# Kernel optimization log

Measured on AMD Instinct MI355X. Metric: run time of the kernel, lower is better.

The kernel has to match this reference:

```python
import jax, jax.numpy as jnp
import numpy as np

D_MODEL = 512
B, S = 8, 1024
NEG_INF = -1e9
EPS = 1e-9


def setup_inputs() -> dict:
    key = jax.random.key(0)
    ks = jax.random.split(key, 6)
    scale = 1.0 / np.sqrt(D_MODEL)
    return {
        "context": jax.random.normal(ks[0], (B, S, D_MODEL), dtype=jnp.float32),
        "eos_mask": jax.random.randint(ks[1], (B, S, S), 0, 2, dtype=jnp.int32),
        "prior": jax.random.uniform(ks[2], (B, S, S), dtype=jnp.float32),
        "Wk": jax.random.normal(ks[3], (D_MODEL, D_MODEL), dtype=jnp.float32) * scale,
        "bk": jnp.zeros((D_MODEL,), dtype=jnp.float32),
        "Wq": jax.random.normal(ks[4], (D_MODEL, D_MODEL), dtype=jnp.float32) * scale,
        "bq": jnp.zeros((D_MODEL,), dtype=jnp.float32),
    }


def reference(context, eos_mask, prior, Wk, bk, Wq, bq):
    seq_len = context.shape[1]
    d_model = context.shape[2]
    # constant structural matrices
    a = jnp.eye(seq_len, k=1, dtype=jnp.int32)          # super-diagonal
    b = jnp.eye(seq_len, k=0, dtype=jnp.int32)          # main diagonal
    c = jnp.eye(seq_len, k=-1, dtype=jnp.int32)         # sub-diagonal
    tri = jnp.triu(jnp.ones((seq_len, seq_len), dtype=jnp.float32))

    # mask = eos_mask & (a + c)   (python precedence: + before &)
    mask = eos_mask & (a + c)                            # [B,S,S] int

    key = context @ Wk.T + bk                            # [B,S,D]
    query = context @ Wq.T + bq                          # [B,S,D]
    scores = jnp.einsum('bqd,bkd->bqk', query, key) / d_model
    scores = jnp.where(mask == 0, NEG_INF, scores)
    neibor_attn = jax.nn.softmax(scores, axis=-1)        # [B,S,S]
    neibor_attn = jnp.sqrt(neibor_attn * jnp.swapaxes(neibor_attn, -2, -1) + EPS)
    neibor_attn = prior + (1.0 - prior) * neibor_attn

    # log-cumsum-exp trick via triangular matmuls (faithful to original)
    t = jnp.where(a == 0, 0.0, jnp.log(neibor_attn + EPS))  # only super-diagonal kept
    t = t @ tri                                           # [B,S,S]
    g_attn = jnp.exp(jnp.einsum('ij,bjk->bik', tri, t))
    g_attn = jnp.where((tri.astype(jnp.int32) - b) == 0, 0.0, g_attn)
    g_attn = g_attn + jnp.swapaxes(g_attn, -2, -1) + jnp.where(b == 0, EPS, neibor_attn)
    return g_attn, neibor_attn
```

## Files before the change

kernel.cpp:

```cpp
#include <hip/hip_runtime.h>
#include <hip/hip_bf16.h>
#include <stdint.h>

#define BB 8
#define SS 1024
#define DD 512
#define MROWS (BB*SS)
#define NCOLS (2*DD)
#define NEG_EPS 1e-9f
#define INV_S (1.0f/1024.0f)

typedef __attribute__((ext_vector_type(8))) __bf16 bf16x8;
typedef __attribute__((ext_vector_type(4))) __bf16 bf16x4;
typedef __attribute__((ext_vector_type(4))) float f32x4;

__device__ __forceinline__ void gload_lds16(const void* g, void* l) {
    __builtin_amdgcn_global_load_lds(
        (const __attribute__((address_space(1))) void*)g,
        (__attribute__((address_space(3))) void*)l,
        16, 0, 0);
}

__global__ __launch_bounds__(256) void f32_to_bf16(const float* __restrict__ src,
                                                   __bf16* __restrict__ dst, int n) {
    int i = (blockIdx.x * blockDim.x + threadIdx.x) * 4;
    int stride = gridDim.x * blockDim.x * 4;
    for (; i < n; i += stride) {
        f32x4 v = *(const f32x4*)(src + i);
        bf16x4 o;
        o[0] = (__bf16)v[0]; o[1] = (__bf16)v[1];
        o[2] = (__bf16)v[2]; o[3] = (__bf16)v[3];
        *(bf16x4*)(dst + i) = o;
    }
}

__global__ __launch_bounds__(256) void gemm_qk(const __bf16* __restrict__ A,
                                               const __bf16* __restrict__ Bt,
                                               const float* __restrict__ bq,
                                               const float* __restrict__ bk,
                                               __bf16* __restrict__ C) {
    __shared__ alignas(16) __bf16 As[128 * 32];
    __shared__ alignas(16) __bf16 Bs[128 * 32];
    const int tid  = threadIdx.x;
    const int lane = tid & 63;
    const int wave = tid >> 6;
    const int wr = wave >> 1, wc = wave & 1;
    const int bm = blockIdx.x & 63, bn = blockIdx.x >> 6;

    f32x4 acc[4][4] = {};
    const int koff = (lane >> 4) * 8;
    const int frow = lane & 15;

    for (int kt = 0; kt < DD; kt += 32) {
        #pragma unroll
        for (int ld = 0; ld < 2; ++ld) {
            int chunk = ld * 256 + tid;
            int row = chunk >> 2;
            int kc  = (chunk & 3) * 8;
            const __bf16* ga = A  + (size_t)(bm * 128 + row) * DD + kt + kc;
            const __bf16* gb = Bt + (size_t)(bn * 128 + row) * DD + kt + kc;
            gload_lds16(ga, (void*)(As + (size_t)(ld * 256 + wave * 64) * 8));
            gload_lds16(gb, (void*)(Bs + (size_t)(ld * 256 + wave * 64) * 8));
        }
        __syncthreads();
        bf16x8 av[4], bv[4];
        #pragma unroll
        for (int m = 0; m < 4; ++m)
            av[m] = *(const bf16x8*)(As + (wr * 64 + m * 16 + frow) * 32 + koff);
        #pragma unroll
        for (int n = 0; n < 4; ++n)
            bv[n] = *(const bf16x8*)(Bs + (wc * 64 + n * 16 + frow) * 32 + koff);
        #pragma unroll
        for (int m = 0; m < 4; ++m)
            #pragma unroll
            for (int n = 0; n < 4; ++n)
                acc[m][n] = __builtin_amdgcn_mfma_f32_16x16x32_bf16(av[m], bv[n], acc[m][n], 0, 0, 0);
        __syncthreads();
    }

    #pragma unroll
    for (int m = 0; m < 4; ++m) {
        int row = bm * 128 + wr * 64 + m * 16 + (lane >> 4) * 4;
        #pragma unroll
        for (int n = 0; n < 4; ++n) {
            int col = bn * 128 + wc * 64 + n * 16 + frow;
            float bias = (col < DD) ? bq[col] : bk[col - DD];
            #pragma unroll
            for (int rg = 0; rg < 4; ++rg) {
                C[(size_t)(row + rg) * NCOLS + col] = (__bf16)(acc[m][n][rg] + bias);
            }
        }
    }
}

__global__ __launch_bounds__(256) void band_softmax(const __bf16* __restrict__ qk,
                                                    const int* __restrict__ eos,
                                                    float* __restrict__ pp,
                                                    float* __restrict__ pm,
                                                    float* __restrict__ uniV) {
    int row  = blockIdx.x * 4 + (threadIdx.x >> 6);
    int lane = threadIdx.x & 63;
    int b = row >> 10, s = row & 1023;

    const __bf16* Qr = qk + (size_t)row * NCOLS;
    bf16x8 qv = *(const bf16x8*)(Qr + lane * 8);

    bool hasP = (s < SS - 1), hasM = (s > 0);
    float sp = 0.f, sm = 0.f;
    if (hasP) {
        bf16x8 kv = *(const bf16x8*)(qk + (size_t)(row + 1) * NCOLS + DD + lane * 8);
        #pragma unroll
        for (int j = 0; j < 8; ++j) sp += (float)qv[j] * (float)kv[j];
    }
    if (hasM) {
        bf16x8 kv = *(const bf16x8*)(qk + (size_t)(row - 1) * NCOLS + DD + lane * 8);
        #pragma unroll
        for (int j = 0; j < 8; ++j) sm += (float)qv[j] * (float)kv[j];
    }
    #pragma unroll
    for (int off = 32; off > 0; off >>= 1) {
        sp += __shfl_xor(sp, off);
        sm += __shfl_xor(sm, off);
    }
    if (lane == 0) {
        float s_plus  = sp * (1.0f / (float)DD);
        float s_minus = sm * (1.0f / (float)DD);
        bool vp = hasP && (eos[(size_t)b * SS * SS + (size_t)s * SS + (s + 1)] != 0);
        bool vm = hasM && (eos[(size_t)b * SS * SS + (size_t)s * SS + (s - 1)] != 0);
        float opp, opm, ouni;
        if (!vp && !vm) {
            opp = INV_S; opm = INV_S; ouni = INV_S;
        } else {
            float mx = -3.0e38f;
            if (vp) mx = s_plus;
            if (vm) mx = fmaxf(mx, s_minus);
            float ep = vp ? __expf(s_plus - mx) : 0.f;
            float em = vm ? __expf(s_minus - mx) : 0.f;
            float inv = 1.f / (ep + em);
            opp = ep * inv; opm = em * inv; ouni = 0.f;
        }
        pp[row] = opp; pm[row] = opm; uniV[row] = ouni;
    }
}

__global__ __launch_bounds__(1024) void scan_kernel(const float* __restrict__ prior,
                                                    const float* __restrict__ pp,
                                                    const float* __restrict__ pm,
                                                    float* __restrict__ Cbuf) {
    int b = blockIdx.x;
    int j = threadIdx.x;
    __shared__ float sb[1024];
    float Lj = 0.f;
    if (j < SS - 1) {
        float pr = prior[((size_t)b * SS + j) * SS + (j + 1)];
        float prod = pp[b * SS + j] * pm[b * SS + j + 1];
        float na = pr + (1.f - pr) * sqrtf(prod + NEG_EPS);
        Lj = __logf(na + NEG_EPS);
    }
    sb[j] = Lj;
    __syncthreads();
    for (int off = 1; off < 1024; off <<= 1) {
        float v = (j >= off) ? sb[j - off] : 0.f;
        __syncthreads();
        sb[j] += v;
        __syncthreads();
    }
    float Cj = (j == 0) ? 0.f : sb[j - 1];
    Cbuf[b * SS + j] = Cj;
}

__global__ __launch_bounds__(256) void fill_kernel(const float* __restrict__ prior,
                                                   const float* __restrict__ pp,
                                                   const float* __restrict__ pm,
                                                   const float* __restrict__ uniV,
                                                   const float* __restrict__ Cbuf,
                                                   float* __restrict__ gout,
                                                   float* __restrict__ naout) {
    int r = blockIdx.x;
    int b = r >> 10, q = r & 1023;
    int k0 = threadIdx.x * 4;
    size_t rowoff = (size_t)r * SS;

    f32x4 pr4 = *(const f32x4*)(prior + rowoff + k0);
    f32x4 uk4 = *(const f32x4*)(uniV + (b << 10) + k0);
    f32x4 C4  = *(const f32x4*)(Cbuf + (b << 10) + k0);
    float uniq = uniV[r];
    float ppq  = pp[r];
    float pmq  = pm[r];
    float Cq   = Cbuf[r];
    float ppp  = (q > 0)      ? pp[r - 1] : 0.f;
    float pmn  = (q < SS - 1) ? pm[r + 1] : 0.f;

    f32x4 g4, na4;
    #pragma unroll
    for (int j = 0; j < 4; ++j) {
        int k = k0 + j;
        float pr = pr4[j];
        float Aqk = (k == q - 1) ? pmq : ((k == q + 1) ? ppq : uniq);
        float Akq = (k == q - 1) ? ppp : ((k == q + 1) ? pmn : uk4[j]);
        float na = pr + (1.f - pr) * sqrtf(Aqk * Akq + NEG_EPS);
        float g;
        if (k == q) {
            g = na;
        } else {
            float dd = (k > q) ? (C4[j] - Cq) : (Cq - C4[j]);
            g = __expf(dd) + NEG_EPS;
        }
        na4[j] = na;
        g4[j]  = g;
    }
    *(f32x4*)(gout + rowoff + k0)  = g4;
    *(f32x4*)(naout + rowoff + k0) = na4;
}

extern "C" void kernel_launch(void* const* d_in, const int* in_sizes, int n_in,
                              void* d_out, int out_size, void* d_ws, size_t ws_size,
                              hipStream_t stream) {
    const float* ctx   = (const float*)d_in[0];
    const int*   eos   = (const int*)d_in[1];
    const float* prior = (const float*)d_in[2];
    const float* Wk    = (const float*)d_in[3];
    const float* bk    = (const float*)d_in[4];
    const float* Wq    = (const float*)d_in[5];
    const float* bq    = (const float*)d_in[6];

    float* gout  = (float*)d_out;
    float* naout = gout + (size_t)BB * SS * SS;

    char* ws = (char*)d_ws;
    __bf16* ctx_bf = (__bf16*)ws;
    __bf16* w_bf   = (__bf16*)(ws + (8u << 20));
    __bf16* qk     = (__bf16*)(ws + (9u << 20));
    float*  ppb    = (float*)(ws + (25u << 20));
    float*  pmb    = ppb + MROWS;
    float*  uniV   = pmb + MROWS;
    float*  Cbuf   = uniV + MROWS;

    f32_to_bf16<<<2048, 256, 0, stream>>>(ctx, ctx_bf, MROWS * DD);
    f32_to_bf16<<<256, 256, 0, stream>>>(Wq, w_bf, DD * DD);
    f32_to_bf16<<<256, 256, 0, stream>>>(Wk, w_bf + DD * DD, DD * DD);

    gemm_qk<<<64 * 8, 256, 0, stream>>>(ctx_bf, w_bf, bq, bk, qk);

    band_softmax<<<MROWS / 4, 256, 0, stream>>>(qk, eos, ppb, pmb, uniV);

    scan_kernel<<<BB, 1024, 0, stream>>>(prior, ppb, pmb, Cbuf);

    fill_kernel<<<MROWS, 256, 0, stream>>>(prior, ppb, pmb, uniV, Cbuf, gout, naout);
}
```

Measured before the change: 169.4 us.

## Reassociate QK scores via precomputed Wq^T Wk and fuse band softmax with scan

```diff
diff --git a/kernel.cpp b/kernel.cpp
--- a/kernel.cpp
+++ b/kernel.cpp
@@ -6,7 +6,6 @@
 #define SS 1024
 #define DD 512
 #define MROWS (BB*SS)
-#define NCOLS (2*DD)
 #define NEG_EPS 1e-9f
 #define INV_S (1.0f/1024.0f)
 
@@ -21,57 +20,117 @@
         16, 0, 0);
 }
 
-__global__ __launch_bounds__(256) void f32_to_bf16(const float* __restrict__ src,
-                                                   __bf16* __restrict__ dst, int n) {
-    int i = (blockIdx.x * blockDim.x + threadIdx.x) * 4;
-    int stride = gridDim.x * blockDim.x * 4;
-    for (; i < n; i += stride) {
-        f32x4 v = *(const f32x4*)(src + i);
-        bf16x4 o;
-        o[0] = (__bf16)v[0]; o[1] = (__bf16)v[1];
-        o[2] = (__bf16)v[2]; o[3] = (__bf16)v[3];
-        *(bf16x4*)(dst + i) = o;
-    }
-}
-
-__global__ __launch_bounds__(256) void gemm_qk(const __bf16* __restrict__ A,
-                                               const __bf16* __restrict__ Bt,
-                                               const float* __restrict__ bq,
-                                               const float* __restrict__ bk,
-                                               __bf16* __restrict__ C) {
-    __shared__ alignas(16) __bf16 As[128 * 32];
+__global__ __launch_bounds__(256) void prep_kernel(const float* __restrict__ ctx,
+                                                   const float* __restrict__ Wq,
+                                                   const float* __restrict__ Wk,
+                                                   const float* __restrict__ bq,
+                                                   const float* __restrict__ bk,
+                                                   __bf16* __restrict__ ctx_bf,
+                                                   __bf16* __restrict__ m_bf,
+                                                   float* __restrict__ avec,
+                                                   float* __restrict__ bvec,
+                                                   float* __restrict__ c0p) {
+    __shared__ float sQ[64 * 32];
+    __shared__ float sK[64 * 32];
+    __shared__ float red[256];
+    const int blk = blockIdx.x;
+    const int t = threadIdx.x;
+
+    if (blk < 2048) {
+        int i = (blk * 256 + t) * 4;
+        const int stride = 2048 * 256 * 4;
+        for (; i < MROWS * DD; i += stride) {
+            f32x4 v = *(const f32x4*)(ctx + i);
+            bf16x4 o;
+            o[0] = (__bf16)v[0]; o[1] = (__bf16)v[1];
+            o[2] = (__bf16)v[2]; o[3] = (__bf16)v[3];
+            *(bf16x4*)(ctx_bf + i) = o;
+        }
+    } else if (blk < 2304) {
+        const int mb = blk - 2048;
+        const int bi = mb >> 4, bj = mb & 15;
+        const int ti = t >> 4, tj = t & 15;
+        float acc00 = 0.f, acc01 = 0.f, acc10 = 0.f, acc11 = 0.f;
+        for (int e0 = 0; e0 < 512; e0 += 64) {
+            const int r = t >> 2, c8 = (t & 3) * 8;
+            #pragma unroll
+            for (int u = 0; u < 2; ++u) {
+                f32x4 vq = *(const f32x4*)(Wq + (size_t)(e0 + r) * 512 + bi * 32 + c8 + u * 4);
+                f32x4 vk = *(const f32x4*)(Wk + (size_t)(e0 + r) * 512 + bj * 32 + c8 + u * 4);
+                *(f32x4*)(sQ + r * 32 + c8 + u * 4) = vq;
+                *(f32x4*)(sK + r * 32 + c8 + u * 4) = vk;
+            }
+            __syncthreads();
+            #pragma unroll 8
+            for (int e = 0; e < 64; ++e) {
+                float q0 = sQ[e * 32 + ti * 2], q1 = sQ[e * 32 + ti * 2 + 1];
+                float k0 = sK[e * 32 + tj * 2], k1 = sK[e * 32 + tj * 2 + 1];
+                acc00 += q0 * k0; acc01 += q0 * k1;
+                acc10 += q1 * k0; acc11 += q1 * k1;
+            }
+            __syncthreads();
+        }
+        const int i0 = bi * 32 + ti * 2, j0 = bj * 32 + tj * 2;
+        m_bf[(size_t)i0 * 512 + j0]         = (__bf16)acc00;
+        m_bf[(size_t)i0 * 512 + j0 + 1]     = (__bf16)acc01;
+        m_bf[(size_t)(i0 + 1) * 512 + j0]   = (__bf16)acc10;
+        m_bf[(size_t)(i0 + 1) * 512 + j0 + 1] = (__bf16)acc11;
+    } else {
+        #pragma unroll
+        for (int h = 0; h < 2; ++h) {
+            const int d = t + h * 256;
+            float a = 0.f, bv = 0.f;
+            for (int e = 0; e < 512; ++e) {
+                a  += Wq[(size_t)e * 512 + d] * bk[e];
+                bv += Wk[(size_t)e * 512 + d] * bq[e];
+            }
+            avec[d] = a; bvec[d] = bv;
+        }
+        red[t] = bq[t] * bk[t] + bq[t + 256] * bk[t + 256];
+        __syncthreads();
+        for (int off = 128; off > 0; off >>= 1) {
+            if (t < off) red[t] += red[t + off];
+            __syncthreads();
+        }
+        if (t == 0) *c0p = red[0];
+    }
+}
+
+__global__ __launch_bounds__(256) void ugemm(const __bf16* __restrict__ A,
+                                             const __bf16* __restrict__ Bt,
+                                             float* __restrict__ U) {
+    __shared__ alignas(16) __bf16 As[64 * 32];
     __shared__ alignas(16) __bf16 Bs[128 * 32];
     const int tid  = threadIdx.x;
     const int lane = tid & 63;
     const int wave = tid >> 6;
     const int wr = wave >> 1, wc = wave & 1;
-    const int bm = blockIdx.x & 63, bn = blockIdx.x >> 6;
-
-    f32x4 acc[4][4] = {};
+    const int bm = blockIdx.x >> 2, bn = blockIdx.x & 3;
+
+    f32x4 acc[2][4] = {};
     const int koff = (lane >> 4) * 8;
     const int frow = lane & 15;
-
-    for (int kt = 0; kt < DD; kt += 32) {
+    const int row = tid >> 2, kc = (tid & 3) * 8;
+
+    for (int kt = 0; kt < 512; kt += 32) {
+        gload_lds16(A + (size_t)(bm * 64 + row) * 512 + kt + kc,
+                    (void*)(As + (size_t)wave * 64 * 8));
         #pragma unroll
         for (int ld = 0; ld < 2; ++ld) {
-            int chunk = ld * 256 + tid;
-            int row = chunk >> 2;
-            int kc  = (chunk & 3) * 8;
-            const __bf16* ga = A  + (size_t)(bm * 128 + row) * DD + kt + kc;
-            const __bf16* gb = Bt + (size_t)(bn * 128 + row) * DD + kt + kc;
-            gload_lds16(ga, (void*)(As + (size_t)(ld * 256 + wave * 64) * 8));
-            gload_lds16(gb, (void*)(Bs + (size_t)(ld * 256 + wave * 64) * 8));
-        }
-        __syncthreads();
-        bf16x8 av[4], bv[4];
-        #pragma unroll
-        for (int m = 0; m < 4; ++m)
-            av[m] = *(const bf16x8*)(As + (wr * 64 + m * 16 + frow) * 32 + koff);
+            const int brow = (ld * 256 + tid) >> 2;
+            gload_lds16(Bt + (size_t)(bn * 128 + brow) * 512 + kt + kc,
+                        (void*)(Bs + (size_t)(ld * 256 + wave * 64) * 8));
+        }
+        __syncthreads();
+        bf16x8 av[2], bv[4];
+        #pragma unroll
+        for (int m = 0; m < 2; ++m)
+            av[m] = *(const bf16x8*)(As + (wr * 32 + m * 16 + frow) * 32 + koff);
         #pragma unroll
         for (int n = 0; n < 4; ++n)
             bv[n] = *(const bf16x8*)(Bs + (wc * 64 + n * 16 + frow) * 32 + koff);
         #pragma unroll
-        for (int m = 0; m < 4; ++m)
+        for (int m = 0; m < 2; ++m)
             #pragma unroll
             for (int n = 0; n < 4; ++n)
                 acc[m][n] = __builtin_amdgcn_mfma_f32_16x16x32_bf16(av[m], bv[n], acc[m][n], 0, 0, 0);
@@ -79,94 +138,98 @@
     }
 
     #pragma unroll
-    for (int m = 0; m < 4; ++m) {
-        int row = bm * 128 + wr * 64 + m * 16 + (lane >> 4) * 4;
+    for (int m = 0; m < 2; ++m) {
+        const int r0 = bm * 64 + wr * 32 + m * 16 + (lane >> 4) * 4;
         #pragma unroll
         for (int n = 0; n < 4; ++n) {
-            int col = bn * 128 + wc * 64 + n * 16 + frow;
-            float bias = (col < DD) ? bq[col] : bk[col - DD];
+            const int col = bn * 128 + wc * 64 + n * 16 + frow;
             #pragma unroll
-            for (int rg = 0; rg < 4; ++rg) {
-                C[(size_t)(row + rg) * NCOLS + col] = (__bf16)(acc[m][n][rg] + bias);
-            }
-        }
-    }
-}
-
-__global__ __launch_bounds__(256) void band_softmax(const __bf16* __restrict__ qk,
-                                                    const int* __restrict__ eos,
-                                                    float* __restrict__ pp,
-                                                    float* __restrict__ pm,
-                                                    float* __restrict__ uniV) {
-    int row  = blockIdx.x * 4 + (threadIdx.x >> 6);
-    int lane = threadIdx.x & 63;
-    int b = row >> 10, s = row & 1023;
-
-    const __bf16* Qr = qk + (size_t)row * NCOLS;
-    bf16x8 qv = *(const bf16x8*)(Qr + lane * 8);
-
-    bool hasP = (s < SS - 1), hasM = (s > 0);
-    float sp = 0.f, sm = 0.f;
+            for (int rg = 0; rg < 4; ++rg)
+                U[(size_t)(r0 + rg) * 512 + col] = acc[m][n][rg];
+        }
+    }
+}
+
+__global__ __launch_bounds__(1024) void band_scan(const float* __restrict__ ctx,
+                                                  const float* __restrict__ U,
+                                                  const float* __restrict__ avec,
+                                                  const float* __restrict__ bvec,
+                                                  const float* __restrict__ c0p,
+                                                  const int* __restrict__ eos,
+                                                  const float* __restrict__ prior,
+                                                  float* __restrict__ pp,
+                                                  float* __restrict__ pm,
+                                                  float* __restrict__ uniV,
+                                                  float* __restrict__ Cbuf) {
+    __shared__ float shB[1024];
+    __shared__ float shP[1024];
+    const int b = blockIdx.x, s = threadIdx.x;
+    const int r = b * SS + s;
+    const bool hasP = (s < SS - 1), hasM = (s > 0);
+    const int rp = hasP ? r + 1 : r;
+    const int rm = hasM ? r - 1 : r;
+
+    const f32x4* cp  = (const f32x4*)(ctx + (size_t)r * DD);
+    const f32x4* Up  = (const f32x4*)(U + (size_t)rp * DD);
+    const f32x4* Um  = (const f32x4*)(U + (size_t)rm * DD);
+    const f32x4* a4  = (const f32x4*)avec;
+    const f32x4* b4  = (const f32x4*)bvec;
+
+    f32x4 aP = {}, aM = {}, aA = {}, aB = {};
+    for (int d = 0; d < DD / 4; ++d) {
+        f32x4 c = cp[d];
+        aP += c * Up[d];
+        aM += c * Um[d];
+        aA += c * a4[d];
+        aB += c * b4[d];
+    }
+    float sp = aP[0] + aP[1] + aP[2] + aP[3];
+    float sm = aM[0] + aM[1] + aM[2] + aM[3];
+    float al = aA[0] + aA[1] + aA[2] + aA[3];
+    float be = aB[0] + aB[1] + aB[2] + aB[3];
+
+    shB[s] = be;
+    __syncthreads();
+    const float c0 = *c0p;
+    const float scp = (sp + al + (hasP ? shB[s + 1] : 0.f) + c0) * (1.f / (float)DD);
+    const float scm = (sm + al + (hasM ? shB[s - 1] : 0.f) + c0) * (1.f / (float)DD);
+
+    const bool vp = hasP && (eos[(size_t)b * SS * SS + (size_t)s * SS + (s + 1)] != 0);
+    const bool vm = hasM && (eos[(size_t)b * SS * SS + (size_t)s * SS + (s - 1)] != 0);
+
+    float opp, opm, ouni;
+    if (!vp && !vm) {
+        opp = INV_S; opm = INV_S; ouni = INV_S;
+    } else {
+        float mx = -3.0e38f;
+        if (vp) mx = scp;
+        if (vm) mx = fmaxf(mx, scm);
+        float ep = vp ? __expf(scp - mx) : 0.f;
+        float em = vm ? __expf(scm - mx) : 0.f;
+        float inv = 1.f / (ep + em);
+        opp = ep * inv; opm = em * inv; ouni = 0.f;
+    }
+    pp[r] = opp; pm[r] = opm; uniV[r] = ouni;
+
+    shP[s] = opm;
+    __syncthreads();
+    float Lj = 0.f;
     if (hasP) {
-        bf16x8 kv = *(const bf16x8*)(qk + (size_t)(row + 1) * NCOLS + DD + lane * 8);
-        #pragma unroll
-        for (int j = 0; j < 8; ++j) sp += (float)qv[j] * (float)kv[j];
-    }
-    if (hasM) {
-        bf16x8 kv = *(const bf16x8*)(qk + (size_t)(row - 1) * NCOLS + DD + lane * 8);
-        #pragma unroll
-        for (int j = 0; j < 8; ++j) sm += (float)qv[j] * (float)kv[j];
-    }
-    #pragma unroll
-    for (int off = 32; off > 0; off >>= 1) {
-        sp += __shfl_xor(sp, off);
-        sm += __shfl_xor(sm, off);
-    }
-    if (lane == 0) {
-        float s_plus  = sp * (1.0f / (float)DD);
-        float s_minus = sm * (1.0f / (float)DD);
-        bool vp = hasP && (eos[(size_t)b * SS * SS + (size_t)s * SS + (s + 1)] != 0);
-        bool vm = hasM && (eos[(size_t)b * SS * SS + (size_t)s * SS + (s - 1)] != 0);
-        float opp, opm, ouni;
-        if (!vp && !vm) {
-            opp = INV_S; opm = INV_S; ouni = INV_S;
-        } else {
-            float mx = -3.0e38f;
-            if (vp) mx = s_plus;
-            if (vm) mx = fmaxf(mx, s_minus);
-            float ep = vp ? __expf(s_plus - mx) : 0.f;
-            float em = vm ? __expf(s_minus - mx) : 0.f;
-            float inv = 1.f / (ep + em);
-            opp = ep * inv; opm = em * inv; ouni = 0.f;
-        }
-        pp[row] = opp; pm[row] = opm; uniV[row] = ouni;
-    }
-}
-
-__global__ __launch_bounds__(1024) void scan_kernel(const float* __restrict__ prior,
-                                                    const float* __restrict__ pp,
-                                                    const float* __restrict__ pm,
-                                                    float* __restrict__ Cbuf) {
-    int b = blockIdx.x;
-    int j = threadIdx.x;
-    __shared__ float sb[1024];
-    float Lj = 0.f;
-    if (j < SS - 1) {
-        float pr = prior[((size_t)b * SS + j) * SS + (j + 1)];
-        float prod = pp[b * SS + j] * pm[b * SS + j + 1];
+        float pr = prior[(size_t)b * SS * SS + (size_t)s * SS + (s + 1)];
+        float prod = opp * shP[s + 1];
         float na = pr + (1.f - pr) * sqrtf(prod + NEG_EPS);
         Lj = __logf(na + NEG_EPS);
     }
-    sb[j] = Lj;
+    __syncthreads();
+    shB[s] = Lj;
     __syncthreads();
     for (int off = 1; off < 1024; off <<= 1) {
-        float v = (j >= off) ? sb[j - off] : 0.f;
-        __syncthreads();
-        sb[j] += v;
-        __syncthreads();
-    }
-    float Cj = (j == 0) ? 0.f : sb[j - 1];
-    Cbuf[b * SS + j] = Cj;
+        float v = (s >= off) ? shB[s - off] : 0.f;
+        __syncthreads();
+        shB[s] += v;
+        __syncthreads();
+    }
+    Cbuf[r] = (s == 0) ? 0.f : shB[s - 1];
 }
 
 __global__ __launch_bounds__(256) void fill_kernel(const float* __restrict__ prior,
@@ -176,10 +239,10 @@
                                                    const float* __restrict__ Cbuf,
                                                    float* __restrict__ gout,
                                                    float* __restrict__ naout) {
-    int r = blockIdx.x;
-    int b = r >> 10, q = r & 1023;
-    int k0 = threadIdx.x * 4;
-    size_t rowoff = (size_t)r * SS;
+    const int r = blockIdx.x;
+    const int b = r >> 10, q = r & 1023;
+    const int k0 = threadIdx.x * 4;
+    const size_t rowoff = (size_t)r * SS;
 
     f32x4 pr4 = *(const f32x4*)(prior + rowoff + k0);
     f32x4 uk4 = *(const f32x4*)(uniV + (b << 10) + k0);
@@ -229,22 +292,18 @@
 
     char* ws = (char*)d_ws;
     __bf16* ctx_bf = (__bf16*)ws;
-    __bf16* w_bf   = (__bf16*)(ws + (8u << 20));
-    __bf16* qk     = (__bf16*)(ws + (9u << 20));
-    float*  ppb    = (float*)(ws + (25u << 20));
+    __bf16* m_bf   = (__bf16*)(ws + (8u << 20));
+    float*  U      = (float*)(ws + (9u << 20));
+    float*  avec   = (float*)(ws + (25u << 20));
+    float*  bvec   = avec + 512;
+    float*  c0p    = bvec + 512;
+    float*  ppb    = (float*)(ws + (26u << 20));
     float*  pmb    = ppb + MROWS;
     float*  uniV   = pmb + MROWS;
     float*  Cbuf   = uniV + MROWS;
 
-    f32_to_bf16<<<2048, 256, 0, stream>>>(ctx, ctx_bf, MROWS * DD);
-    f32_to_bf16<<<256, 256, 0, stream>>>(Wq, w_bf, DD * DD);
-    f32_to_bf16<<<256, 256, 0, stream>>>(Wk, w_bf + DD * DD, DD * DD);
-
-    gemm_qk<<<64 * 8, 256, 0, stream>>>(ctx_bf, w_bf, bq, bk, qk);
-
-    band_softmax<<<MROWS / 4, 256, 0, stream>>>(qk, eos, ppb, pmb, uniV);
-
-    scan_kernel<<<BB, 1024, 0, stream>>>(prior, ppb, pmb, Cbuf);
-
+    prep_kernel<<<2305, 256, 0, stream>>>(ctx, Wq, Wk, bq, bk, ctx_bf, m_bf, avec, bvec, c0p);
+    ugemm<<<512, 256, 0, stream>>>(ctx_bf, m_bf, U);
+    band_scan<<<BB, 1024, 0, stream>>>(ctx, U, avec, bvec, c0p, eos, prior, ppb, pmb, uniV, Cbuf);
     fill_kernel<<<MROWS, 256, 0, stream>>>(prior, ppb, pmb, uniV, Cbuf, gout, naout);
 }
```

After: 421.0 us. +148.5%, slower.
